# Optimization experiments

Measured on AMD Instinct MI355X. Metric: run time of the kernel, lower is better.

The kernel has to match this reference:

```python
import jax, jax.numpy as jnp
import numpy as np

B, T, D = 4, 2048, 1024
H = 16
HD = D // H


def setup_inputs() -> dict:
    key = jax.random.key(0)
    ks = jax.random.split(key, 6)
    s = 1.0 / np.sqrt(D)
    return {
        "inputs": jax.random.normal(ks[0], (B, T, D), dtype=jnp.float32),
        "Wq": jax.random.normal(ks[1], (D, D), dtype=jnp.float32) * s,
        "Wk": jax.random.normal(ks[2], (D, D), dtype=jnp.float32) * s,
        "Wv": jax.random.normal(ks[3], (D, D), dtype=jnp.float32) * s,
        "Wo": jax.random.normal(ks[4], (D, D), dtype=jnp.float32) * s,
        "bo": jax.random.normal(ks[5], (D,), dtype=jnp.float32) * 0.01,
    }


def reference(inputs, Wq, Wk, Wv, Wo, bo):
    # qkv projections (torch Linear: x @ W.T; here W stored as [in, out])
    q = jnp.einsum('btd,de->bte', inputs, Wq).reshape(B, T, H, HD)
    k = jnp.einsum('btd,de->bte', inputs, Wk).reshape(B, T, H, HD)
    v = jnp.einsum('btd,de->bte', inputs, Wv).reshape(B, T, H, HD)
    # scores [B,H,T,T]
    scores = jnp.einsum('bqhd,bkhd->bhqk', q, k)
    causal = jnp.triu(jnp.ones((T, T), dtype=bool), k=1)
    scores = jnp.where(causal, -jnp.inf, scores)
    attn = jax.nn.softmax(scores / jnp.sqrt(jnp.float32(HD)), axis=-1)
    ctx = jnp.einsum('bhqk,bkhd->bqhd', attn, v).reshape(B, T, D)
    return jnp.einsum('btd,de->bte', ctx, Wo) + bo
```

## Files before the change

kernel.cpp:

```cpp
#include <hip/hip_runtime.h>

typedef unsigned short u16;
typedef __attribute__((ext_vector_type(8))) __bf16 bf16x8;
typedef __attribute__((ext_vector_type(4))) float f32x4;

#define B_  4
#define T_  2048
#define D_  1024
#define H_  16
#define HD_ 64
#define M_  (B_*T_)

__device__ __forceinline__ u16 f2bf(float x) {
  unsigned u = __float_as_uint(x);
  return (u16)((u + 0x7FFFu + ((u >> 16) & 1u)) >> 16);
}

__device__ __forceinline__ void async16(const void* g, void* lds) {
  __builtin_amdgcn_global_load_lds((__attribute__((address_space(1))) void*)g,
                                   (__attribute__((address_space(3))) void*)lds,
                                   16, 0, 0);
}

__global__ void k_convert_x(const float* __restrict__ x, u16* __restrict__ xb) {
  const int n4 = M_ * D_ / 4;
  for (int i = blockIdx.x * blockDim.x + threadIdx.x; i < n4; i += gridDim.x * blockDim.x) {
    float4 v = ((const float4*)x)[i];
    u16 o0 = f2bf(v.x), o1 = f2bf(v.y), o2 = f2bf(v.z), o3 = f2bf(v.w);
    unsigned lo = (unsigned)o0 | ((unsigned)o1 << 16);
    unsigned hi = (unsigned)o2 | ((unsigned)o3 << 16);
    ((uint2*)xb)[i] = make_uint2(lo, hi);
  }
}

__global__ void k_transpose_w(const float* __restrict__ Wq, const float* __restrict__ Wk,
                              const float* __restrict__ Wv, const float* __restrict__ Wo,
                              u16* __restrict__ WqT, u16* __restrict__ WkT,
                              u16* __restrict__ WvT, u16* __restrict__ WoT) {
  __shared__ float tile[32][33];
  const float* W; u16* Wt;
  switch (blockIdx.z) {
    case 0:  W = Wq; Wt = WqT; break;
    case 1:  W = Wk; Wt = WkT; break;
    case 2:  W = Wv; Wt = WvT; break;
    default: W = Wo; Wt = WoT; break;
  }
  int tx = threadIdx.x & 31, ty = threadIdx.x >> 5;
  int k0 = blockIdx.y * 32, n0 = blockIdx.x * 32;
#pragma unroll
  for (int i = 0; i < 4; i++) {
    int r = ty + i * 8;
    tile[r][tx] = W[(k0 + r) * D_ + n0 + tx];
  }
  __syncthreads();
#pragma unroll
  for (int i = 0; i < 4; i++) {
    int r = ty + i * 8;
    Wt[(n0 + r) * D_ + k0 + tx] = f2bf(tile[tx][r]);
  }
}

__device__ __forceinline__ void gemm_tile(const u16* __restrict__ A, const u16* __restrict__ Bt,
                                          u16* Alds, u16* Blds,
                                          int m0, int n0, f32x4 acc[4][4]) {
  const int tid = threadIdx.x;
  const int l = tid & 63, w = tid >> 6;
  const int wm = (w >> 1) * 64, wn = (w & 1) * 64;
  const int lr = l & 15, lg = l >> 4;
  const f32x4 fz = {0.f, 0.f, 0.f, 0.f};
#pragma unroll
  for (int i = 0; i < 4; i++)
#pragma unroll
    for (int j = 0; j < 4; j++) acc[i][j] = fz;

  for (int kt = 0; kt < 1024; kt += 64) {
    __syncthreads();
#pragma unroll
    for (int i = 0; i < 4; i++) {
      int ch = tid + 256 * i;
      int r = ch >> 3, c8 = ch & 7;
      async16(A  + (m0 + r) * 1024 + kt + c8 * 8, Alds + ch * 8);
      async16(Bt + (n0 + r) * 1024 + kt + c8 * 8, Blds + ch * 8);
    }
    __syncthreads();
#pragma unroll
    for (int kk = 0; kk < 64; kk += 32) {
      bf16x8 af[4], bfr[4];
#pragma unroll
      for (int mi = 0; mi < 4; mi++)
        af[mi] = *(const bf16x8*)(Alds + (wm + mi * 16 + lr) * 64 + kk + lg * 8);
#pragma unroll
      for (int ni = 0; ni < 4; ni++)
        bfr[ni] = *(const bf16x8*)(Blds + (wn + ni * 16 + lr) * 64 + kk + lg * 8);
#pragma unroll
      for (int mi = 0; mi < 4; mi++)
#pragma unroll
        for (int ni = 0; ni < 4; ni++)
          acc[mi][ni] = __builtin_amdgcn_mfma_f32_16x16x32_bf16(af[mi], bfr[ni], acc[mi][ni], 0, 0, 0);
    }
  }
}

__device__ __forceinline__ void gemm_swz(int& m0, int& n0) {
  int lin = blockIdx.x + blockIdx.y * 8;
  int swz = (lin & 7) * 64 + (lin >> 3);
  m0 = (swz >> 3) * 128;
  n0 = (swz & 7) * 128;
}

__global__ __launch_bounds__(256) void k_gemm_qkv(const u16* __restrict__ X,
                                                  const u16* __restrict__ WqT, const u16* __restrict__ WkT,
                                                  const u16* __restrict__ WvT,
                                                  u16* __restrict__ Q, u16* __restrict__ K, u16* __restrict__ V) {
  __shared__ u16 Alds[128 * 64];
  __shared__ u16 Blds[128 * 64];
  const u16* Bt; u16* Out;
  switch (blockIdx.z) {
    case 0:  Bt = WqT; Out = Q; break;
    case 1:  Bt = WkT; Out = K; break;
    default: Bt = WvT; Out = V; break;
  }
  int m0, n0;
  gemm_swz(m0, n0);
  f32x4 acc[4][4];
  gemm_tile(X, Bt, Alds, Blds, m0, n0, acc);
  const int l = threadIdx.x & 63, w = threadIdx.x >> 6;
  const int wm = (w >> 1) * 64, wn = (w & 1) * 64;
  const int lr = l & 15, lg = l >> 4;
#pragma unroll
  for (int mi = 0; mi < 4; mi++)
#pragma unroll
    for (int ni = 0; ni < 4; ni++)
#pragma unroll
      for (int r = 0; r < 4; r++) {
        int row = m0 + wm + mi * 16 + lg * 4 + r;
        int col = n0 + wn + ni * 16 + lr;
        Out[row * D_ + col] = f2bf(acc[mi][ni][r]);
      }
}

__global__ __launch_bounds__(256) void k_gemm_out(const u16* __restrict__ Cx, const u16* __restrict__ WoT,
                                                  const float* __restrict__ bo, float* __restrict__ out) {
  __shared__ u16 Alds[128 * 64];
  __shared__ u16 Blds[128 * 64];
  int m0, n0;
  gemm_swz(m0, n0);
  f32x4 acc[4][4];
  gemm_tile(Cx, WoT, Alds, Blds, m0, n0, acc);
  const int l = threadIdx.x & 63, w = threadIdx.x >> 6;
  const int wm = (w >> 1) * 64, wn = (w & 1) * 64;
  const int lr = l & 15, lg = l >> 4;
#pragma unroll
  for (int mi = 0; mi < 4; mi++)
#pragma unroll
    for (int ni = 0; ni < 4; ni++)
#pragma unroll
      for (int r = 0; r < 4; r++) {
        int row = m0 + wm + mi * 16 + lg * 4 + r;
        int col = n0 + wn + ni * 16 + lr;
        out[row * D_ + col] = acc[mi][ni][r] + bo[col];
      }
}

__global__ void k_transpose_v(const u16* __restrict__ V, u16* __restrict__ Vt) {
  __shared__ u16 tile[64][65];
  int bh = blockIdx.y;
  int b = bh >> 4, h = bh & 15;
  int t0 = blockIdx.x * 64;
  int tx = threadIdx.x & 63, ty = threadIdx.x >> 6;
#pragma unroll
  for (int i = 0; i < 16; i++) {
    int r = ty + i * 4;
    tile[r][tx] = V[(b * T_ + t0 + r) * D_ + h * HD_ + tx];
  }
  __syncthreads();
#pragma unroll
  for (int i = 0; i < 16; i++) {
    int d = ty + i * 4;
    Vt[((size_t)(bh * HD_ + d)) * T_ + t0 + tx] = tile[tx][d];
  }
}

__global__ __launch_bounds__(256) void k_flash(const u16* __restrict__ Q, const u16* __restrict__ Kb,
                                               const u16* __restrict__ Vt, u16* __restrict__ ctx) {
  __shared__ u16 Klds[64 * 64];
  __shared__ u16 Vlds[64 * 64];
  __shared__ u16 Plds[4][32 * 64];
  int lin = blockIdx.x + blockIdx.y * gridDim.x;
  int swz = (lin & 7) * 128 + (lin >> 3);
  const int qb = swz & 15, bh = swz >> 4;
  const int b = bh >> 4, h = bh & 15;
  const int qs = qb * 128;
  const int tid = threadIdx.x, l = tid & 63, w = tid >> 6;
  const int lr = l & 15, lg = l >> 4, l7 = lr & 7;
  const float EA = 0.18033688f, EB = -17.312340f;

  bf16x8 aQ[2][2];
#pragma unroll
  for (int m = 0; m < 2; m++) {
    const u16* Qrow = Q + (size_t)(b * T_ + qs + w * 32 + m * 16 + lr) * D_ + h * HD_;
    aQ[m][0] = *(const bf16x8*)(Qrow + lg * 8);
    aQ[m][1] = *(const bf16x8*)(Qrow + 32 + lg * 8);
  }

  f32x4 o[2][4];
  float psum[2][4];
  const f32x4 fz = {0.f, 0.f, 0.f, 0.f};
#pragma unroll
  for (int m = 0; m < 2; m++)
#pragma unroll
    for (int i = 0; i < 4; i++) { o[m][i] = fz; psum[m][i] = 0.f; }

  u16* Pw = &Plds[w][0];
  const int wrow = qs + w * 32;

  for (int kv0 = 0; kv0 <= qs + 64; kv0 += 64) {
    __syncthreads();
#pragma unroll
    for (int i = 0; i < 2; i++) {
      int ch = tid + 256 * i;
      int r = ch >> 3, c8 = (ch & 7) ^ (r & 7);
      async16(Kb + (size_t)(b * T_ + kv0 + r) * D_ + h * HD_ + c8 * 8, Klds + ch * 8);
      async16(Vt + (size_t)(bh * HD_ + r) * T_ + kv0 + c8 * 8, Vlds + ch * 8);
    }
    __syncthreads();

    if (kv0 > wrow + 31) continue;

    f32x4 sc[2][4];
#pragma unroll
    for (int m = 0; m < 2; m++)
#pragma unroll
      for (int ni = 0; ni < 4; ni++) sc[m][ni] = fz;
#pragma unroll
    for (int ni = 0; ni < 4; ni++) {
      const int krow = (ni * 16 + lr) * 64;
      bf16x8 bk0 = *(const bf16x8*)(Klds + krow + ((0 + lg) ^ l7) * 8);
      bf16x8 bk1 = *(const bf16x8*)(Klds + krow + ((4 + lg) ^ l7) * 8);
#pragma unroll
      for (int m = 0; m < 2; m++) {
        sc[m][ni] = __builtin_amdgcn_mfma_f32_16x16x32_bf16(aQ[m][0], bk0, sc[m][ni], 0, 0, 0);
        sc[m][ni] = __builtin_amdgcn_mfma_f32_16x16x32_bf16(aQ[m][1], bk1, sc[m][ni], 0, 0, 0);
      }
    }

    const bool anymask = (kv0 + 63 > wrow);
#pragma unroll
    for (int m = 0; m < 2; m++) {
      const int rowb = wrow + m * 16 + lg * 4;
      const int pr0 = m * 16 + lg * 4;
#pragma unroll
      for (int ni = 0; ni < 4; ni++) {
        const int col = kv0 + ni * 16 + lr;
#pragma unroll
        for (int r = 0; r < 4; r++) {
          float x = sc[m][ni][r];
          float e = exp2f(fmaf(x, EA, EB));
          if (anymask && col > rowb + r) e = 0.f;
          psum[m][r] += e;
          int pr = pr0 + r;
          Pw[pr * 64 + (((ni * 2) + (lr >> 3)) ^ (pr & 7)) * 8 + l7] = f2bf(e);
        }
      }
    }

#pragma unroll
    for (int kk2 = 0; kk2 < 2; kk2++) {
      bf16x8 aP[2];
#pragma unroll
      for (int m = 0; m < 2; m++)
        aP[m] = *(const bf16x8*)(Pw + (m * 16 + lr) * 64 + ((kk2 * 4 + lg) ^ l7) * 8);
#pragma unroll
      for (int di = 0; di < 4; di++) {
        bf16x8 bv = *(const bf16x8*)(Vlds + (di * 16 + lr) * 64 + ((kk2 * 4 + lg) ^ l7) * 8);
#pragma unroll
        for (int m = 0; m < 2; m++)
          o[m][di] = __builtin_amdgcn_mfma_f32_16x16x32_bf16(aP[m], bv, o[m][di], 0, 0, 0);
      }
    }
  }

#pragma unroll
  for (int off = 1; off < 16; off <<= 1)
#pragma unroll
    for (int m = 0; m < 2; m++)
#pragma unroll
      for (int r = 0; r < 4; r++)
        psum[m][r] += __shfl_xor(psum[m][r], off, 64);

#pragma unroll
  for (int m = 0; m < 2; m++) {
    float inv[4];
#pragma unroll
    for (int r = 0; r < 4; r++) inv[r] = 1.f / psum[m][r];
#pragma unroll
    for (int di = 0; di < 4; di++)
#pragma unroll
      for (int r = 0; r < 4; r++) {
        int row = b * T_ + qs + w * 32 + m * 16 + lg * 4 + r;
        int col = h * HD_ + di * 16 + lr;
        ctx[(size_t)row * D_ + col] = f2bf(o[m][di][r] * inv[r]);
      }
  }
}

extern "C" void kernel_launch(void* const* d_in, const int* in_sizes, int n_in,
                              void* d_out, int out_size, void* d_ws, size_t ws_size,
                              hipStream_t stream) {
  const float* x  = (const float*)d_in[0];
  const float* Wq = (const float*)d_in[1];
  const float* Wk = (const float*)d_in[2];
  const float* Wv = (const float*)d_in[3];
  const float* Wo = (const float*)d_in[4];
  const float* bo = (const float*)d_in[5];
  float* out = (float*)d_out;

  char* ws = (char*)d_ws;
  u16* Xb  = (u16*)(ws);
  u16* WqT = (u16*)(ws + 16777216);
  u16* WkT = (u16*)(ws + 18874368);
  u16* WvT = (u16*)(ws + 20971520);
  u16* WoT = (u16*)(ws + 23068672);
  u16* Qb  = (u16*)(ws + 25165824);
  u16* Kb  = (u16*)(ws + 41943040);
  u16* Vb  = (u16*)(ws + 58720256);
  u16* Vtb = (u16*)(ws + 75497472);
  u16* Cb  = (u16*)(ws + 92274688);

  k_convert_x<<<dim3(2048), dim3(256), 0, stream>>>(x, Xb);
  k_transpose_w<<<dim3(32, 32, 4), dim3(256), 0, stream>>>(Wq, Wk, Wv, Wo, WqT, WkT, WvT, WoT);
  k_gemm_qkv<<<dim3(8, 64, 3), dim3(256), 0, stream>>>(Xb, WqT, WkT, WvT, Qb, Kb, Vb);
  k_transpose_v<<<dim3(32, 64), dim3(256), 0, stream>>>(Vb, Vtb);
  k_flash<<<dim3(16, 64), dim3(256), 0, stream>>>(Qb, Kb, Vtb, Cb);
  k_gemm_out<<<dim3(8, 64), dim3(256), 0, stream>>>(Cb, WoT, bo, out);
}
```

Measured before the change: 328.5 us.

## Rework flash attention with 32x32 MFMA and register-resident P via permlane swap

The attention kernel switches from 16x16x32 MFMA tiles with P staged through shared memory to 32x32x16 MFMA tiles. It computes S transposed (K as the A operand), packs the probabilities to bf16 with v_cvt_pk_bf16_f32, and reshuffles them with v_permlane32_swap so they feed the PV MFMA straight from registers. This removes the per-wave P LDS buffer and its write and read traffic and simplifies the row-sum reduction. Separately, the Q/K/V weights are packed into one concatenated matrix so a single 2D GEMM grid covers all three projections, and the block-swizzle mapping is dropped from both GEMMs, which may change L2 locality.

```diff
diff --git a/kernel.cpp b/kernel.cpp
--- a/kernel.cpp
+++ b/kernel.cpp
@@ -3,6 +3,7 @@
 typedef unsigned short u16;
 typedef __attribute__((ext_vector_type(8))) __bf16 bf16x8;
 typedef __attribute__((ext_vector_type(4))) float f32x4;
+typedef __attribute__((ext_vector_type(16))) float f32x16;
 
 #define B_  4
 #define T_  2048
@@ -14,6 +15,12 @@
 __device__ __forceinline__ u16 f2bf(float x) {
   unsigned u = __float_as_uint(x);
   return (u16)((u + 0x7FFFu + ((u >> 16) & 1u)) >> 16);
+}
+
+__device__ __forceinline__ unsigned cvtpk(float lo, float hi) {
+  unsigned r;
+  asm("v_cvt_pk_bf16_f32 %0, %1, %2" : "=v"(r) : "v"(lo), "v"(hi));
+  return r;
 }
 
 __device__ __forceinline__ void async16(const void* g, void* lds) {
@@ -35,15 +42,14 @@
 
 __global__ void k_transpose_w(const float* __restrict__ Wq, const float* __restrict__ Wk,
                               const float* __restrict__ Wv, const float* __restrict__ Wo,
-                              u16* __restrict__ WqT, u16* __restrict__ WkT,
-                              u16* __restrict__ WvT, u16* __restrict__ WoT) {
+                              u16* __restrict__ WqkvT, u16* __restrict__ WoT) {
   __shared__ float tile[32][33];
   const float* W; u16* Wt;
   switch (blockIdx.z) {
-    case 0:  W = Wq; Wt = WqT; break;
-    case 1:  W = Wk; Wt = WkT; break;
-    case 2:  W = Wv; Wt = WvT; break;
-    default: W = Wo; Wt = WoT; break;
+    case 0:  W = Wq; Wt = WqkvT;               break;
+    case 1:  W = Wk; Wt = WqkvT + 1024 * D_;   break;
+    case 2:  W = Wv; Wt = WqkvT + 2048 * D_;   break;
+    default: W = Wo; Wt = WoT;                 break;
   }
   int tx = threadIdx.x & 31, ty = threadIdx.x >> 5;
   int k0 = blockIdx.y * 32, n0 = blockIdx.x * 32;
@@ -101,29 +107,17 @@
   }
 }
 
-__device__ __forceinline__ void gemm_swz(int& m0, int& n0) {
-  int lin = blockIdx.x + blockIdx.y * 8;
-  int swz = (lin & 7) * 64 + (lin >> 3);
-  m0 = (swz >> 3) * 128;
-  n0 = (swz & 7) * 128;
-}
-
 __global__ __launch_bounds__(256) void k_gemm_qkv(const u16* __restrict__ X,
-                                                  const u16* __restrict__ WqT, const u16* __restrict__ WkT,
-                                                  const u16* __restrict__ WvT,
+                                                  const u16* __restrict__ WqkvT,
                                                   u16* __restrict__ Q, u16* __restrict__ K, u16* __restrict__ V) {
   __shared__ u16 Alds[128 * 64];
   __shared__ u16 Blds[128 * 64];
-  const u16* Bt; u16* Out;
-  switch (blockIdx.z) {
-    case 0:  Bt = WqT; Out = Q; break;
-    case 1:  Bt = WkT; Out = K; break;
-    default: Bt = WvT; Out = V; break;
-  }
-  int m0, n0;
-  gemm_swz(m0, n0);
+  int m0 = blockIdx.y * 128, n0 = blockIdx.x * 128;
+  int reg = n0 >> 10;
+  u16* Out = (reg == 0) ? Q : (reg == 1) ? K : V;
+  int nb = n0 & 1023;
   f32x4 acc[4][4];
-  gemm_tile(X, Bt, Alds, Blds, m0, n0, acc);
+  gemm_tile(X, WqkvT, Alds, Blds, m0, n0, acc);
   const int l = threadIdx.x & 63, w = threadIdx.x >> 6;
   const int wm = (w >> 1) * 64, wn = (w & 1) * 64;
   const int lr = l & 15, lg = l >> 4;
@@ -134,7 +128,7 @@
 #pragma unroll
       for (int r = 0; r < 4; r++) {
         int row = m0 + wm + mi * 16 + lg * 4 + r;
-        int col = n0 + wn + ni * 16 + lr;
+        int col = nb + wn + ni * 16 + lr;
         Out[row * D_ + col] = f2bf(acc[mi][ni][r]);
       }
 }
@@ -143,8 +137,7 @@
                                                   const float* __restrict__ bo, float* __restrict__ out) {
   __shared__ u16 Alds[128 * 64];
   __shared__ u16 Blds[128 * 64];
-  int m0, n0;
-  gemm_swz(m0, n0);
+  int m0 = blockIdx.y * 128, n0 = blockIdx.x * 128;
   f32x4 acc[4][4];
   gemm_tile(Cx, WoT, Alds, Blds, m0, n0, acc);
   const int l = threadIdx.x & 63, w = threadIdx.x >> 6;
@@ -185,34 +178,25 @@
                                                const u16* __restrict__ Vt, u16* __restrict__ ctx) {
   __shared__ u16 Klds[64 * 64];
   __shared__ u16 Vlds[64 * 64];
-  __shared__ u16 Plds[4][32 * 64];
   int lin = blockIdx.x + blockIdx.y * gridDim.x;
   int swz = (lin & 7) * 128 + (lin >> 3);
   const int qb = swz & 15, bh = swz >> 4;
   const int b = bh >> 4, h = bh & 15;
   const int qs = qb * 128;
   const int tid = threadIdx.x, l = tid & 63, w = tid >> 6;
-  const int lr = l & 15, lg = l >> 4, l7 = lr & 7;
+  const int q5 = l & 31, hi = l >> 5;
+  const int wrow = qs + w * 32;
+  const int qa = wrow + q5;
   const float EA = 0.18033688f, EB = -17.312340f;
 
-  bf16x8 aQ[2][2];
-#pragma unroll
-  for (int m = 0; m < 2; m++) {
-    const u16* Qrow = Q + (size_t)(b * T_ + qs + w * 32 + m * 16 + lr) * D_ + h * HD_;
-    aQ[m][0] = *(const bf16x8*)(Qrow + lg * 8);
-    aQ[m][1] = *(const bf16x8*)(Qrow + 32 + lg * 8);
-  }
-
-  f32x4 o[2][4];
-  float psum[2][4];
-  const f32x4 fz = {0.f, 0.f, 0.f, 0.f};
-#pragma unroll
-  for (int m = 0; m < 2; m++)
-#pragma unroll
-    for (int i = 0; i < 4; i++) { o[m][i] = fz; psum[m][i] = 0.f; }
-
-  u16* Pw = &Plds[w][0];
-  const int wrow = qs + w * 32;
+  const u16* Qrow = Q + (size_t)(b * T_ + qa) * D_ + h * HD_;
+  bf16x8 aQ[4];
+#pragma unroll
+  for (int kc = 0; kc < 4; kc++)
+    aQ[kc] = *(const bf16x8*)(Qrow + kc * 16 + hi * 8);
+
+  f32x16 o[2] = {};
+  float psum = 0.f;
 
   for (int kv0 = 0; kv0 <= qs + 64; kv0 += 64) {
     __syncthreads();
@@ -226,82 +210,58 @@
     __syncthreads();
 
     if (kv0 > wrow + 31) continue;
-
-    f32x4 sc[2][4];
-#pragma unroll
-    for (int m = 0; m < 2; m++)
-#pragma unroll
-      for (int ni = 0; ni < 4; ni++) sc[m][ni] = fz;
-#pragma unroll
-    for (int ni = 0; ni < 4; ni++) {
-      const int krow = (ni * 16 + lr) * 64;
-      bf16x8 bk0 = *(const bf16x8*)(Klds + krow + ((0 + lg) ^ l7) * 8);
-      bf16x8 bk1 = *(const bf16x8*)(Klds + krow + ((4 + lg) ^ l7) * 8);
-#pragma unroll
-      for (int m = 0; m < 2; m++) {
-        sc[m][ni] = __builtin_amdgcn_mfma_f32_16x16x32_bf16(aQ[m][0], bk0, sc[m][ni], 0, 0, 0);
-        sc[m][ni] = __builtin_amdgcn_mfma_f32_16x16x32_bf16(aQ[m][1], bk1, sc[m][ni], 0, 0, 0);
-      }
-    }
-
     const bool anymask = (kv0 + 63 > wrow);
-#pragma unroll
-    for (int m = 0; m < 2; m++) {
-      const int rowb = wrow + m * 16 + lg * 4;
-      const int pr0 = m * 16 + lg * 4;
-#pragma unroll
-      for (int ni = 0; ni < 4; ni++) {
-        const int col = kv0 + ni * 16 + lr;
-#pragma unroll
-        for (int r = 0; r < 4; r++) {
-          float x = sc[m][ni][r];
-          float e = exp2f(fmaf(x, EA, EB));
-          if (anymask && col > rowb + r) e = 0.f;
-          psum[m][r] += e;
-          int pr = pr0 + r;
-          Pw[pr * 64 + (((ni * 2) + (lr >> 3)) ^ (pr & 7)) * 8 + l7] = f2bf(e);
+
+#pragma unroll
+    for (int kt = 0; kt < 2; kt++) {
+      f32x16 st = {};
+#pragma unroll
+      for (int kc = 0; kc < 4; kc++) {
+        const int row = kt * 32 + q5;
+        bf16x8 kf = *(const bf16x8*)(Klds + row * 64 + (((kc * 2 + hi) ^ (row & 7))) * 8);
+        st = __builtin_amdgcn_mfma_f32_32x32x16_bf16(kf, aQ[kc], st, 0, 0, 0);
+      }
+      float e[16];
+#pragma unroll
+      for (int r = 0; r < 16; r++) {
+        int kva = kv0 + kt * 32 + (r & 3) + 8 * (r >> 2) + 4 * hi;
+        float ev = exp2f(fmaf(st[r], EA, EB));
+        if (anymask && kva > qa) ev = 0.f;
+        e[r] = ev;
+        psum += ev;
+      }
+#pragma unroll
+      for (int eh = 0; eh < 2; eh++) {
+        unsigned a0 = cvtpk(e[eh * 8 + 0], e[eh * 8 + 1]);
+        unsigned a1 = cvtpk(e[eh * 8 + 2], e[eh * 8 + 3]);
+        unsigned b0 = cvtpk(e[eh * 8 + 4], e[eh * 8 + 5]);
+        unsigned b1 = cvtpk(e[eh * 8 + 6], e[eh * 8 + 7]);
+        asm volatile("v_permlane32_swap_b32 %0, %1" : "+v"(a0), "+v"(b0));
+        asm volatile("v_permlane32_swap_b32 %0, %1" : "+v"(a1), "+v"(b1));
+        union { unsigned u[4]; bf16x8 v; } pf;
+        pf.u[0] = a0; pf.u[1] = a1; pf.u[2] = b0; pf.u[3] = b1;
+        const int ch = kt * 4 + eh * 2 + hi;
+#pragma unroll
+        for (int dt = 0; dt < 2; dt++) {
+          const int vrow = dt * 32 + q5;
+          bf16x8 vf = *(const bf16x8*)(Vlds + vrow * 64 + ((ch ^ (vrow & 7))) * 8);
+          o[dt] = __builtin_amdgcn_mfma_f32_32x32x16_bf16(vf, pf.v, o[dt], 0, 0, 0);
         }
       }
     }
-
-#pragma unroll
-    for (int kk2 = 0; kk2 < 2; kk2++) {
-      bf16x8 aP[2];
-#pragma unroll
-      for (int m = 0; m < 2; m++)
-        aP[m] = *(const bf16x8*)(Pw + (m * 16 + lr) * 64 + ((kk2 * 4 + lg) ^ l7) * 8);
-#pragma unroll
-      for (int di = 0; di < 4; di++) {
-        bf16x8 bv = *(const bf16x8*)(Vlds + (di * 16 + lr) * 64 + ((kk2 * 4 + lg) ^ l7) * 8);
-#pragma unroll
-        for (int m = 0; m < 2; m++)
-          o[m][di] = __builtin_amdgcn_mfma_f32_16x16x32_bf16(aP[m], bv, o[m][di], 0, 0, 0);
-      }
-    }
-  }
-
-#pragma unroll
-  for (int off = 1; off < 16; off <<= 1)
-#pragma unroll
-    for (int m = 0; m < 2; m++)
-#pragma unroll
-      for (int r = 0; r < 4; r++)
-        psum[m][r] += __shfl_xor(psum[m][r], off, 64);
-
-#pragma unroll
-  for (int m = 0; m < 2; m++) {
-    float inv[4];
-#pragma unroll
-    for (int r = 0; r < 4; r++) inv[r] = 1.f / psum[m][r];
-#pragma unroll
-    for (int di = 0; di < 4; di++)
-#pragma unroll
-      for (int r = 0; r < 4; r++) {
-        int row = b * T_ + qs + w * 32 + m * 16 + lg * 4 + r;
-        int col = h * HD_ + di * 16 + lr;
-        ctx[(size_t)row * D_ + col] = f2bf(o[m][di][r] * inv[r]);
-      }
-  }
+  }
+
+  psum += __shfl_xor(psum, 32, 64);
+  const float inv = 1.f / psum;
+  u16* crow = ctx + (size_t)(b * T_ + qa) * D_ + h * HD_;
+#pragma unroll
+  for (int dt = 0; dt < 2; dt++)
+#pragma unroll
+    for (int r = 0; r < 16; r += 2) {
+      int d = dt * 32 + (r & 3) + 8 * (r >> 2) + 4 * hi;
+      unsigned pk2 = cvtpk(o[dt][r] * inv, o[dt][r + 1] * inv);
+      *(unsigned*)(crow + d) = pk2;
+    }
 }
 
 extern "C" void kernel_launch(void* const* d_in, const int* in_sizes, int n_in,
@@ -316,20 +276,18 @@
   float* out = (float*)d_out;
 
   char* ws = (char*)d_ws;
-  u16* Xb  = (u16*)(ws);
-  u16* WqT = (u16*)(ws + 16777216);
-  u16* WkT = (u16*)(ws + 18874368);
-  u16* WvT = (u16*)(ws + 20971520);
-  u16* WoT = (u16*)(ws + 23068672);
-  u16* Qb  = (u16*)(ws + 25165824);
-  u16* Kb  = (u16*)(ws + 41943040);
-  u16* Vb  = (u16*)(ws + 58720256);
-  u16* Vtb = (u16*)(ws + 75497472);
-  u16* Cb  = (u16*)(ws + 92274688);
+  u16* Xb     = (u16*)(ws);
+  u16* WqkvT  = (u16*)(ws + 16777216);
+  u16* WoT    = (u16*)(ws + 23068672);
+  u16* Qb     = (u16*)(ws + 25165824);
+  u16* Kb     = (u16*)(ws + 41943040);
+  u16* Vb     = (u16*)(ws + 58720256);
+  u16* Vtb    = (u16*)(ws + 75497472);
+  u16* Cb     = (u16*)(ws + 92274688);
 
   k_convert_x<<<dim3(2048), dim3(256), 0, stream>>>(x, Xb);
-  k_transpose_w<<<dim3(32, 32, 4), dim3(256), 0, stream>>>(Wq, Wk, Wv, Wo, WqT, WkT, WvT, WoT);
-  k_gemm_qkv<<<dim3(8, 64, 3), dim3(256), 0, stream>>>(Xb, WqT, WkT, WvT, Qb, Kb, Vb);
+  k_transpose_w<<<dim3(32, 32, 4), dim3(256), 0, stream>>>(Wq, Wk, Wv, Wo, WqkvT, WoT);
+  k_gemm_qkv<<<dim3(24, 64), dim3(256), 0, stream>>>(Xb, WqkvT, Qb, Kb, Vb);
   k_transpose_v<<<dim3(32, 64), dim3(256), 0, stream>>>(Vb, Vtb);
   k_flash<<<dim3(16, 64), dim3(256), 0, stream>>>(Qb, Kb, Vtb, Cb);
   k_gemm_out<<<dim3(8, 64), dim3(256), 0, stream>>>(Cb, WoT, bo, out);
```

New measurement: 312.0 us. 5.0% less time.
